# Kernel optimization log

Measured on AMD Instinct MI355X. Metric: run time of the kernel, lower is better.

Reference implementation:

```python
import jax, jax.numpy as jnp
import numpy as np

N = 100000
E = 1600000
IN_C, HID, HEADS, OUT_C = 128, 64, 4, 2
NEG_SLOPE = 0.2


def setup_inputs() -> dict:
    key = jax.random.key(0)
    ks = jax.random.split(key, 10)
    def glorot(k, shape):
        fan = shape[0] + shape[-1]
        return jax.random.uniform(k, shape, jnp.float32, -1.0, 1.0) * np.sqrt(6.0 / fan)
    x = jax.random.normal(ks[0], (N, IN_C), jnp.float32)
    edge_index = jax.random.randint(ks[1], (2, E), 0, N, jnp.int64)
    return {
        "x": x,
        "edge_index": edge_index,
        "W1": glorot(ks[2], (IN_C, HID)),
        "b1": jnp.zeros((HID,), jnp.float32),
        "W2": glorot(ks[3], (HID, HEADS * HID)),
        "att_src": glorot(ks[4], (HEADS, HID)) ,
        "att_dst": glorot(ks[5], (HEADS, HID)),
        "b2": jnp.zeros((HEADS * HID,), jnp.float32),
        "W3": glorot(ks[6], (HEADS * HID, OUT_C)),
        "b3": jnp.zeros((OUT_C,), jnp.float32),
    }


def _add_self_loops(edge_index, n):
    loop = jnp.arange(n, dtype=edge_index.dtype)
    src = jnp.concatenate([edge_index[0], loop])
    dst = jnp.concatenate([edge_index[1], loop])
    return src, dst


def gcn_conv(x, W, b, src, dst, n):
    # x' = X W, then symmetric deg-normalized scatter-add (self-loops included)
    xw = x @ W
    deg = jax.ops.segment_sum(jnp.ones_like(dst, dtype=xw.dtype), dst, num_segments=n)
    dinv = jnp.where(deg > 0, jax.lax.rsqrt(deg), 0.0)
    norm = dinv[src] * dinv[dst]                      # [E2]
    out = jax.ops.segment_sum(xw[src] * norm[:, None], dst, num_segments=n)
    return out + b


def gat_conv(x, W, att_src, att_dst, b, src, dst, n, heads, ch):
    xw = (x @ W).reshape(n, heads, ch)                # [N, H, C]
    a_s = (xw * att_src).sum(-1)                      # [N, H]
    a_d = (xw * att_dst).sum(-1)
    e = jax.nn.leaky_relu(a_s[src] + a_d[dst], NEG_SLOPE)   # [E2, H]
    # segment softmax over incoming edges per destination node
    m = jax.ops.segment_max(e, dst, num_segments=n)
    m = jnp.where(jnp.isfinite(m), m, 0.0)
    e = jnp.exp(e - m[dst])
    den = jax.ops.segment_sum(e, dst, num_segments=n)
    alpha = e / (den[dst] + 1e-16)                    # [E2, H]
    out = jax.ops.segment_sum(xw[src] * alpha[:, :, None], dst, num_segments=n)
    return out.reshape(n, heads * ch) + b


def reference(x, edge_index, W1, b1, W2, att_src, att_dst, b2, W3, b3):
    n = x.shape[0]
    src, dst = _add_self_loops(edge_index, n)
    h = jax.nn.relu(gcn_conv(x, W1, b1, src, dst, n))
    h = jax.nn.elu(gat_conv(h, W2, att_src, att_dst, b2, src, dst, n, HEADS, HID))
    return gcn_conv(h, W3, b3, src, dst, n)
```

## Files before the change

kernel.cpp:

```cpp
#include <hip/hip_runtime.h>
#include <math.h>

#define N_NODES 100000
#define N_EDGES 1600000
#define E2      (N_NODES + N_EDGES)
#define IN_C    128
#define HID     64
#define HEADS   4
#define HH      256
#define OUT_C   2
#define NEG_SLOPE 0.2f

#define SB   1024
#define NSB  ((N_NODES + SB - 1) / SB)
#define NRANGE 4
#define RDIV   25000
#define BINS   RDIV
#define BINW   (BINS / 2)
#define NBK    100
#define CHUNK  (N_EDGES / NBK)
#define C4     (CHUNK / 4)
#define CITER4 ((C4 + 255) / 256)
#define NHB    (NRANGE * NBK)
#define NFC    (N_EDGES / 256)
#define RT     10
#define NT1    6250
#define NGEMM1 ((NT1 + 3) / 4)

typedef __attribute__((ext_vector_type(8))) short bf16x8;
typedef __attribute__((ext_vector_type(4))) float f32x4;

__device__ __forceinline__ float bf2f(unsigned short u) {
    return __uint_as_float(((unsigned)u) << 16);
}
__device__ __forceinline__ unsigned short f2bf(float f) {
    unsigned u = __float_as_uint(f);
    u += 0x7fffu + ((u >> 16) & 1u);
    return (unsigned short)(u >> 16);
}


__global__ __launch_bounds__(256) void k_prep(const float* __restrict__ W2,
        const float* __restrict__ W1,
        const float* __restrict__ att_src, const float* __restrict__ att_dst,
        unsigned short* __restrict__ W2t, unsigned short* __restrict__ wsdt,
        unsigned short* __restrict__ W1t) {
    int b = blockIdx.x, t = threadIdx.x;
    if (b < 64) {
        int g = b * 256 + t;
        int k = g >> 8, n = g & 255;
        W2t[n * 64 + k] = f2bf(W2[g]);
        return;
    }
    if (b < 66) {
        int g = (b - 64) * 256 + t;
        wsdt[512 + g] = 0;
        int k = g >> 3, o = g & 7;
        int h = o & 3;
        const float* att = (o < 4) ? att_src : att_dst;
        float acc = 0.f;
        const float* wrow = W2 + (size_t)k * HH + h * 64;
        const float* arow = att + h * 64;
        for (int c = 0; c < 64; ++c) acc = fmaf(wrow[c], arow[c], acc);
        wsdt[o * 64 + k] = f2bf(acc);
        return;
    }
    int g = (b - 66) * 256 + t;
    int k = g >> 6, n = g & 63;
    W1t[n * 128 + k] = f2bf(W1[g]);
}

__global__ __launch_bounds__(256) void k_hist(const int* __restrict__ ei,
        unsigned short* __restrict__ hp16, unsigned short* __restrict__ rank16) {
    __shared__ unsigned int hh[BINW];
    int b = blockIdx.x, t = threadIdx.x;
    int r = b & 3, k = b >> 2;
    for (int i = t; i < BINW; i += 256) hh[i] = 0u;
    __syncthreads();
    const int4* dp4 = (const int4*)(ei + N_EDGES + (size_t)k * CHUNK);
    unsigned short* rp = rank16 + (size_t)k * CHUNK;
    int lo = r * RDIV;
#pragma unroll 2
    for (int it = 0; it < CITER4; ++it) {
        int i4 = it * 256 + t;
        if (i4 < C4) {
            int4 v = dp4[i4];
            int base = i4 * 4;
            int d0 = v.x - lo, d1 = v.y - lo, d2 = v.z - lo, d3 = v.w - lo;
            if ((unsigned)d0 < (unsigned)RDIV) {
                unsigned sh = (d0 & 1) * 16;
                unsigned old = atomicAdd(&hh[d0 >> 1], 1u << sh);
                rp[base + 0] = (unsigned short)(old >> sh);
            }
            if ((unsigned)d1 < (unsigned)RDIV) {
                unsigned sh = (d1 & 1) * 16;
                unsigned old = atomicAdd(&hh[d1 >> 1], 1u << sh);
                rp[base + 1] = (unsigned short)(old >> sh);
            }
            if ((unsigned)d2 < (unsigned)RDIV) {
                unsigned sh = (d2 & 1) * 16;
                unsigned old = atomicAdd(&hh[d2 >> 1], 1u << sh);
                rp[base + 2] = (unsigned short)(old >> sh);
            }
            if ((unsigned)d3 < (unsigned)RDIV) {
                unsigned sh = (d3 & 1) * 16;
                unsigned old = atomicAdd(&hh[d3 >> 1], 1u << sh);
                rp[base + 3] = (unsigned short)(old >> sh);
            }
        }
    }
    __syncthreads();
    unsigned* hp = (unsigned*)(hp16 + (size_t)(r * NBK + k) * BINS);
    for (int i = t; i < BINW; i += 256) hp[i] = hh[i];
}

__global__ __launch_bounds__(256) void k_scan1(unsigned short* __restrict__ hp16,
        int* __restrict__ cnt, int* __restrict__ bsum) {
    int b = blockIdx.x, t = threadIdx.x;
    int s = 0;
#pragma unroll
    for (int u = 0; u < 4; ++u) {
        int i = b * SB + u * 256 + t;
        if (i < N_NODES) {
            int r = i / RDIV, bin = i - r * RDIV;
            unsigned short* p = hp16 + (size_t)r * NBK * BINS + bin;
            unsigned acc = 0;
            for (int k = 0; k < NBK; ++k) {
                unsigned short hv = p[(size_t)k * BINS];
                p[(size_t)k * BINS] = (unsigned short)acc;
                acc += hv;
            }
            cnt[i] = (int)acc;
            s += (int)acc + 1;
        }
    }
#pragma unroll
    for (int off = 1; off < 64; off <<= 1) s += __shfl_xor(s, off);
    __shared__ int wsum[4];
    int lane = t & 63, wv = t >> 6;
    if (lane == 0) wsum[wv] = s;
    __syncthreads();
    if (t == 0) bsum[b] = (wsum[0] + wsum[1]) + (wsum[2] + wsum[3]);
}

__global__ __launch_bounds__(256) void k_scan3(const int* __restrict__ cnt,
        const int* __restrict__ bsum, int* __restrict__ rowptr,
        float* __restrict__ dinv, int* __restrict__ col) {
    int b = blockIdx.x, t = threadIdx.x;
    int lane = t & 63, wv = t >> 6;
    __shared__ int wred[4];
    {
        int v = (t < b) ? bsum[t] : 0;
#pragma unroll
        for (int off = 1; off < 64; off <<= 1) v += __shfl_xor(v, off);
        if (lane == 0) wred[wv] = v;
    }
    __syncthreads();
    int pre = (wred[0] + wred[1]) + (wred[2] + wred[3]);
    __syncthreads();

    int i = b * SB + t * 4;
    int c0 = 0, c1 = 0, c2 = 0, c3 = 0;
    if (i + 3 < N_NODES) {
        int4 v = *(const int4*)(cnt + i);
        c0 = v.x; c1 = v.y; c2 = v.z; c3 = v.w;
    } else if (i < N_NODES) {
        c0 = cnt[i];
        if (i + 1 < N_NODES) c1 = cnt[i + 1];
        if (i + 2 < N_NODES) c2 = cnt[i + 2];
    }
    int n0 = (i < N_NODES), n1 = (i + 1 < N_NODES),
        n2 = (i + 2 < N_NODES), n3 = (i + 3 < N_NODES);
    int d0 = c0 + n0, d1 = c1 + n1, d2 = c2 + n2, d3 = c3 + n3;
    int s = (d0 + d1) + (d2 + d3);
    int inc = s;
#pragma unroll
    for (int off = 1; off < 64; off <<= 1) {
        int u = __shfl_up(inc, off);
        if (lane >= off) inc += u;
    }
    __shared__ int wtot[4];
    if (lane == 63) wtot[wv] = inc;
    __syncthreads();
    int base = pre + (inc - s);
    for (int w = 0; w < wv; ++w) base += wtot[w];
    if (n0) { rowptr[i]     = base;                dinv[i]     = rsqrtf((float)d0); col[base] = i; }
    if (n1) { rowptr[i + 1] = base + d0;           dinv[i + 1] = rsqrtf((float)d1); col[base + d0] = i + 1; }
    if (n2) { rowptr[i + 2] = base + d0 + d1;      dinv[i + 2] = rsqrtf((float)d2); col[base + d0 + d1] = i + 2; }
    if (n3) { rowptr[i + 3] = base + d0 + d1 + d2; dinv[i + 3] = rsqrtf((float)d3); col[base + d0 + d1 + d2] = i + 3; }
    if (b == 0 && t == 0) rowptr[N_NODES] = E2;
}

__global__ __launch_bounds__(256) void k_fillg(const int* __restrict__ ei,
        const int* __restrict__ rowptr, const unsigned short* __restrict__ hp16,
        const unsigned short* __restrict__ rank16, int* __restrict__ col,
        const float* __restrict__ x, const unsigned short* __restrict__ W1t,
        unsigned short* __restrict__ xw1b) {
    int b = blockIdx.x, t = threadIdx.x;
    if (b < NGEMM1) {
        int lane = t & 63, wv = t >> 6;
        int m = lane & 15, quad = lane >> 4;
        bf16x8 B[4][4];
#pragma unroll
        for (int ct = 0; ct < 4; ++ct)
#pragma unroll
            for (int ks = 0; ks < 4; ++ks)
                B[ct][ks] = *(const bf16x8*)(W1t + (size_t)(ct * 16 + m) * IN_C
                                             + ks * 32 + quad * 8);
        int tile = b * 4 + wv;
        if (tile >= NT1) return;
        int rbase = tile * 16;
        const float* xp = x + (size_t)(rbase + m) * IN_C + quad * 8;
        f32x4 c0 = {0.f, 0.f, 0.f, 0.f}, c1 = c0, c2 = c0, c3 = c0;
#pragma unroll
        for (int ks = 0; ks < 4; ++ks) {
            float4 f0 = *(const float4*)(xp + ks * 32);
            float4 f1 = *(const float4*)(xp + ks * 32 + 4);
            bf16x8 a;
            a[0] = (short)f2bf(f0.x); a[1] = (short)f2bf(f0.y);
            a[2] = (short)f2bf(f0.z); a[3] = (short)f2bf(f0.w);
            a[4] = (short)f2bf(f1.x); a[5] = (short)f2bf(f1.y);
            a[6] = (short)f2bf(f1.z); a[7] = (short)f2bf(f1.w);
            c0 = __builtin_amdgcn_mfma_f32_16x16x32_bf16(a, B[0][ks], c0, 0, 0, 0);
            c1 = __builtin_amdgcn_mfma_f32_16x16x32_bf16(a, B[1][ks], c1, 0, 0, 0);
            c2 = __builtin_amdgcn_mfma_f32_16x16x32_bf16(a, B[2][ks], c2, 0, 0, 0);
            c3 = __builtin_amdgcn_mfma_f32_16x16x32_bf16(a, B[3][ks], c3, 0, 0, 0);
        }
        int row0 = rbase + quad * 4;
#pragma unroll
        for (int ct = 0; ct < 4; ++ct) {
            f32x4 c = (ct == 0) ? c0 : (ct == 1) ? c1 : (ct == 2) ? c2 : c3;
            unsigned short* p = xw1b + (size_t)row0 * HID + ct * 16 + m;
#pragma unroll
            for (int r = 0; r < 4; ++r) p[(size_t)r * HID] = f2bf(c[r]);
        }
        return;
    }
    int i = (b - NGEMM1) * 256 + t;
    int d = ei[N_EDGES + i];
    int s = ei[i];
    int r = d / RDIV;
    int bin = d - r * RDIV;
    int k = i / CHUNK;
    unsigned pos = (unsigned)rowptr[d] + 1u
                 + (unsigned)hp16[(size_t)(r * NBK + k) * BINS + bin]
                 + (unsigned)rank16[i];
    col[pos] = s;
}

__global__ __launch_bounds__(256) void k_agg1(const int* __restrict__ rowptr,
        const int* __restrict__ col, const unsigned short* __restrict__ xw1b,
        const float* __restrict__ dinv, const float* __restrict__ b1,
        unsigned short* __restrict__ h1b) {
    int t = threadIdx.x;
    int lane = t & 63;
    int d = blockIdx.x * 4 + (t >> 6);
    if (d >= N_NODES) return;
    int start = rowptr[d], end = rowptr[d + 1];
    int sub = lane >> 4;
    int cpos = lane & 15;
    float4 acc = make_float4(0.f, 0.f, 0.f, 0.f);
    for (int base = start; base < end; base += 64) {
        int cnt = min(64, end - base);
        int sl = (base + lane < end) ? col[base + lane] : 0;
#pragma unroll 2
        for (int j = 0; j < cnt; j += 4) {
            int idx = j + sub;
            int sj = __shfl(sl, idx);
            if (idx < cnt) {
                float di = dinv[sj];
                ushort4 v = ((const ushort4*)(xw1b + (size_t)sj * HID))[cpos];
                acc.x = fmaf(di, bf2f(v.x), acc.x);
                acc.y = fmaf(di, bf2f(v.y), acc.y);
                acc.z = fmaf(di, bf2f(v.z), acc.z);
                acc.w = fmaf(di, bf2f(v.w), acc.w);
            }
        }
    }
    acc.x += __shfl_xor(acc.x, 16); acc.y += __shfl_xor(acc.y, 16);
    acc.z += __shfl_xor(acc.z, 16); acc.w += __shfl_xor(acc.w, 16);
    acc.x += __shfl_xor(acc.x, 32); acc.y += __shfl_xor(acc.y, 32);
    acc.z += __shfl_xor(acc.z, 32); acc.w += __shfl_xor(acc.w, 32);
    if (lane < 16) {
        float di = dinv[d];
        float4 b = ((const float4*)b1)[lane];
        float ox = fmaf(acc.x, di, b.x); ox = ox > 0.f ? ox : 0.f;
        float oy = fmaf(acc.y, di, b.y); oy = oy > 0.f ? oy : 0.f;
        float oz = fmaf(acc.z, di, b.z); oz = oz > 0.f ? oz : 0.f;
        float ow = fmaf(acc.w, di, b.w); ow = ow > 0.f ? ow : 0.f;
        ushort4 o = make_ushort4(f2bf(ox), f2bf(oy), f2bf(oz), f2bf(ow));
        ((ushort4*)(h1b + (size_t)d * HID))[lane] = o;
    }
}

__global__ __launch_bounds__(256) void k_attn(const unsigned short* __restrict__ h1b,
        const unsigned short* __restrict__ wsdt,
        float* __restrict__ a_s, float* __restrict__ a_d) {
    int t = threadIdx.x;
    int lane = t & 63, wv = t >> 6;
    int m = lane & 15, quad = lane >> 4;
    bf16x8 Bw0 = *(const bf16x8*)(wsdt + (size_t)m * 64 + quad * 8);
    bf16x8 Bw1 = *(const bf16x8*)(wsdt + (size_t)m * 64 + 32 + quad * 8);
    int tile = blockIdx.x * 4 + wv;
    if (tile >= NT1) return;
    int rbase = tile * 16;
    const unsigned short* ap = h1b + (size_t)(rbase + m) * 64 + quad * 8;
    bf16x8 a0 = *(const bf16x8*)(ap);
    bf16x8 a1 = *(const bf16x8*)(ap + 32);
    f32x4 aw = {0.f, 0.f, 0.f, 0.f};
    aw = __builtin_amdgcn_mfma_f32_16x16x32_bf16(a0, Bw0, aw, 0, 0, 0);
    aw = __builtin_amdgcn_mfma_f32_16x16x32_bf16(a1, Bw1, aw, 0, 0, 0);
    int row = rbase + quad * 4;
    if (m < 4) {
#pragma unroll
        for (int r = 0; r < 4; ++r) a_s[(row + r) * 4 + m] = aw[r];
    } else if (m < 8) {
#pragma unroll
        for (int r = 0; r < 4; ++r) a_d[(row + r) * 4 + (m - 4)] = aw[r];
    }
}

__global__ __launch_bounds__(256) void k_agg2u(const int* __restrict__ rowptr,
        const int* __restrict__ col, const unsigned short* __restrict__ h1b,
        const float* __restrict__ a_s, const float* __restrict__ a_d,
        unsigned short* __restrict__ ub, int dbase) {
    __shared__ int   ss[4][64];
    __shared__ float sp[4][64][4];
    int t = threadIdx.x;
    int lane = t & 63, wv = t >> 6;
    int d = dbase + blockIdx.x * 4 + wv;
    if (d >= N_NODES) return;
    const float4* as4 = (const float4*)a_s;
    float4 adv = ((const float4*)a_d)[d];
    int start = rowptr[d], end = rowptr[d + 1];

    float den0 = 0.f, den1 = 0.f, den2 = 0.f, den3 = 0.f;
    float acc0 = 0.f, acc1 = 0.f, acc2 = 0.f, acc3 = 0.f;
    for (int base = start; base < end; base += 64) {
        int cnt = min(64, end - base);
        float p0 = 0.f, p1 = 0.f, p2 = 0.f, p3 = 0.f;
        int s = 0;
        if (lane < cnt) {
            s = col[base + lane];
            float4 av = as4[s];
            float v;
            v = av.x + adv.x; v = v > 0.f ? v : NEG_SLOPE * v; p0 = __expf(v);
            v = av.y + adv.y; v = v > 0.f ? v : NEG_SLOPE * v; p1 = __expf(v);
            v = av.z + adv.z; v = v > 0.f ? v : NEG_SLOPE * v; p2 = __expf(v);
            v = av.w + adv.w; v = v > 0.f ? v : NEG_SLOPE * v; p3 = __expf(v);
            den0 += p0; den1 += p1; den2 += p2; den3 += p3;
        }
        ss[wv][lane] = s;
        ((float4*)sp[wv])[lane] = make_float4(p0, p1, p2, p3);
#pragma unroll 4
        for (int j = 0; j < cnt; ++j) {
            int sj = ss[wv][j];
            float4 pj = ((const float4*)sp[wv])[j];
            float v = bf2f(h1b[(unsigned)sj * 64u + (unsigned)lane]);
            acc0 = fmaf(pj.x, v, acc0);
            acc1 = fmaf(pj.y, v, acc1);
            acc2 = fmaf(pj.z, v, acc2);
            acc3 = fmaf(pj.w, v, acc3);
        }
    }
#pragma unroll
    for (int mk = 1; mk < 64; mk <<= 1) {
        den0 += __shfl_xor(den0, mk);
        den1 += __shfl_xor(den1, mk);
        den2 += __shfl_xor(den2, mk);
        den3 += __shfl_xor(den3, mk);
    }
    float u0 = acc0 / (den0 + 1e-16f);
    float u1 = acc1 / (den1 + 1e-16f);
    float u2 = acc2 / (den2 + 1e-16f);
    float u3 = acc3 / (den3 + 1e-16f);
    unsigned short* up = ub + (size_t)d * HH;
    up[lane]       = f2bf(u0);
    up[64 + lane]  = f2bf(u1);
    up[128 + lane] = f2bf(u2);
    up[192 + lane] = f2bf(u3);
}

__global__ __launch_bounds__(256) void k_gemm3m(const unsigned short* __restrict__ ub,
        const unsigned short* __restrict__ W2t, const float* __restrict__ b2,
        const float* __restrict__ W3, const float* __restrict__ dinv,
        float2* __restrict__ xw3) {
    int t = threadIdx.x;
    int lane = t & 63, wv = t >> 6;
    int m = lane & 15, quad = lane >> 4;
    int nb = wv * 64 + m;
    bf16x8 B[4][2];
#pragma unroll
    for (int ct = 0; ct < 4; ++ct)
#pragma unroll
        for (int ks = 0; ks < 2; ++ks)
            B[ct][ks] = *(const bf16x8*)(W2t + (size_t)(nb + ct * 16) * 64
                                         + ks * 32 + quad * 8);
    float bv[4]; float2 w3v[4];
#pragma unroll
    for (int ct = 0; ct < 4; ++ct) {
        int n = nb + ct * 16;
        bv[ct] = b2[n];
        w3v[ct] = ((const float2*)W3)[n];
    }
    __shared__ float red[4][16][2];
    int r0 = blockIdx.x * (RT * 16);
    for (int tile = 0; tile < RT; ++tile) {
        int rbase = r0 + tile * 16;
        const unsigned short* ap = ub + (size_t)(rbase + m) * HH + wv * 64 + quad * 8;
        bf16x8 a0 = *(const bf16x8*)(ap);
        bf16x8 a1 = *(const bf16x8*)(ap + 32);
        f32x4 c0 = {0.f, 0.f, 0.f, 0.f}, c1 = c0, c2 = c0, c3 = c0;
        c0 = __builtin_amdgcn_mfma_f32_16x16x32_bf16(a0, B[0][0], c0, 0, 0, 0);
        c1 = __builtin_amdgcn_mfma_f32_16x16x32_bf16(a0, B[1][0], c1, 0, 0, 0);
        c2 = __builtin_amdgcn_mfma_f32_16x16x32_bf16(a0, B[2][0], c2, 0, 0, 0);
        c3 = __builtin_amdgcn_mfma_f32_16x16x32_bf16(a0, B[3][0], c3, 0, 0, 0);
        c0 = __builtin_amdgcn_mfma_f32_16x16x32_bf16(a1, B[0][1], c0, 0, 0, 0);
        c1 = __builtin_amdgcn_mfma_f32_16x16x32_bf16(a1, B[1][1], c1, 0, 0, 0);
        c2 = __builtin_amdgcn_mfma_f32_16x16x32_bf16(a1, B[2][1], c2, 0, 0, 0);
        c3 = __builtin_amdgcn_mfma_f32_16x16x32_bf16(a1, B[3][1], c3, 0, 0, 0);
        float px[4] = {0.f, 0.f, 0.f, 0.f}, py[4] = {0.f, 0.f, 0.f, 0.f};
#pragma unroll
        for (int ct = 0; ct < 4; ++ct) {
            f32x4 c = (ct == 0) ? c0 : (ct == 1) ? c1 : (ct == 2) ? c2 : c3;
#pragma unroll
            for (int r = 0; r < 4; ++r) {
                float o = c[r] + bv[ct];
                o = o > 0.f ? o : expm1f(o);
                px[r] = fmaf(o, w3v[ct].x, px[r]);
                py[r] = fmaf(o, w3v[ct].y, py[r]);
            }
        }
#pragma unroll
        for (int mk = 1; mk < 16; mk <<= 1) {
#pragma unroll
            for (int r = 0; r < 4; ++r) {
                px[r] += __shfl_xor(px[r], mk);
                py[r] += __shfl_xor(py[r], mk);
            }
        }
        if (m == 0) {
#pragma unroll
            for (int r = 0; r < 4; ++r) {
                red[wv][quad * 4 + r][0] = px[r];
                red[wv][quad * 4 + r][1] = py[r];
            }
        }
        __syncthreads();
        if (t < 32) {
            int row = t >> 1, xy = t & 1;
            float s = red[0][row][xy] + red[1][row][xy]
                    + red[2][row][xy] + red[3][row][xy];
            ((float*)(xw3 + (rbase + row)))[xy] = s * dinv[rbase + row];
        }
        __syncthreads();
    }
}

__global__ __launch_bounds__(256) void k_agg3(const int* __restrict__ rowptr,
        const int* __restrict__ col, const float2* __restrict__ xw3,
        const float* __restrict__ dinv, const float* __restrict__ b3,
        float* __restrict__ out) {
    int t = threadIdx.x;
    int lane = t & 63;
    int g = lane >> 2, s = lane & 3;
    int d = blockIdx.x * 64 + (t >> 6) * 16 + g;
    if (d >= N_NODES) return;
    int e0 = rowptr[d], e1 = rowptr[d + 1];
    float a0 = 0.f, a1 = 0.f;
    for (int e = e0 + s; e < e1; e += 4) {
        float2 v = xw3[col[e]];
        a0 += v.x; a1 += v.y;
    }
    a0 += __shfl_xor(a0, 1); a1 += __shfl_xor(a1, 1);
    a0 += __shfl_xor(a0, 2); a1 += __shfl_xor(a1, 2);
    if (s == 0) {
        float di = dinv[d];
        out[d * 2 + 0] = fmaf(a0, di, b3[0]);
        out[d * 2 + 1] = fmaf(a1, di, b3[1]);
    }
}


extern "C" void kernel_launch(void* const* d_in, const int* in_sizes, int n_in,
                              void* d_out, int out_size, void* d_ws, size_t ws_size,
                              hipStream_t stream) {
    const float* x       = (const float*)d_in[0];
    const int*   ei      = (const int*)d_in[1];
    const float* W1      = (const float*)d_in[2];
    const float* b1      = (const float*)d_in[3];
    const float* W2      = (const float*)d_in[4];
    const float* att_src = (const float*)d_in[5];
    const float* att_dst = (const float*)d_in[6];
    const float* b2      = (const float*)d_in[7];
    const float* W3      = (const float*)d_in[8];
    const float* b3      = (const float*)d_in[9];
    float* out = (float*)d_out;
    (void)in_sizes; (void)n_in; (void)out_size; (void)ws_size;

    char* ws = (char*)d_ws;
    size_t off = 0;
    auto alloc = [&](size_t bytes) -> void* {
        void* p = ws + off;
        off = (off + bytes + 255) & ~(size_t)255;
        return p;
    };
    int*    rowptr = (int*)alloc((N_NODES + 1) * sizeof(int));
    int*    cnt    = (int*)alloc(N_NODES * sizeof(int));
    int*    bsum   = (int*)alloc(NSB * sizeof(int));
    int*    col    = (int*)alloc((size_t)E2 * sizeof(int));
    float*  dinv   = (float*)alloc(N_NODES * sizeof(float));
    unsigned short* W2t  = (unsigned short*)alloc(64 * 256 * sizeof(unsigned short));
    unsigned short* wsdt = (unsigned short*)alloc(16 * 64 * sizeof(unsigned short));
    unsigned short* W1t  = (unsigned short*)alloc(64 * 128 * sizeof(unsigned short));
    unsigned short* xw1b = (unsigned short*)alloc((size_t)N_NODES * HID * sizeof(unsigned short));
    unsigned short* h1b  = (unsigned short*)alloc((size_t)N_NODES * HID * sizeof(unsigned short));
    float*  a_s    = (float*)alloc((size_t)N_NODES * HEADS * sizeof(float));
    float*  a_d    = (float*)alloc((size_t)N_NODES * HEADS * sizeof(float));
    unsigned short* ub   = (unsigned short*)alloc((size_t)N_NODES * HH * sizeof(unsigned short));
    float2* xw3    = (float2*)alloc((size_t)N_NODES * sizeof(float2));
    unsigned short* hp16   = ub;
    unsigned short* rank16 = ub + (size_t)NHB * BINS;

    k_prep<<<98, 256, 0, stream>>>(W2, W1, att_src, att_dst, W2t, wsdt, W1t);
    k_hist<<<NHB, 256, 0, stream>>>(ei, hp16, rank16);
    k_scan1<<<NSB, 256, 0, stream>>>(hp16, cnt, bsum);
    k_scan3<<<NSB, 256, 0, stream>>>(cnt, bsum, rowptr, dinv, col);
    k_fillg<<<NGEMM1 + NFC, 256, 0, stream>>>(ei, rowptr, hp16, rank16,
                                              col, x, W1t, xw1b);

    k_agg1<<<(N_NODES + 3) / 4, 256, 0, stream>>>(rowptr, col, xw1b, dinv, b1, h1b);
    k_attn<<<(NT1 + 3) / 4, 256, 0, stream>>>(h1b, wsdt, a_s, a_d);
    const int HALF = 50000;
    k_agg2u<<<HALF / 4, 256, 0, stream>>>(rowptr, col, h1b, a_s, a_d, ub, 0);
    k_agg2u<<<(N_NODES - HALF + 3) / 4, 256, 0, stream>>>(rowptr, col, h1b, a_s, a_d, ub, HALF);
    k_gemm3m<<<(N_NODES / 16) / RT, 256, 0, stream>>>(ub, W2t, b2, W3, dinv, xw3);
    k_agg3<<<(N_NODES + 63) / 64, 256, 0, stream>>>(rowptr, col, xw3, dinv, b3, out);
}
```

Measured before the change: 370.9 us.

## Move GEMM1 into scan kernel and vectorize GAT aggregation gathers

After: 387.4 us. 1.04x slower.

```diff
diff --git a/kernel.cpp b/kernel.cpp
--- a/kernel.cpp
+++ b/kernel.cpp
@@ -114,90 +114,12 @@
     for (int i = t; i < BINW; i += 256) hp[i] = hh[i];
 }
 
-__global__ __launch_bounds__(256) void k_scan1(unsigned short* __restrict__ hp16,
-        int* __restrict__ cnt, int* __restrict__ bsum) {
-    int b = blockIdx.x, t = threadIdx.x;
-    int s = 0;
-#pragma unroll
-    for (int u = 0; u < 4; ++u) {
-        int i = b * SB + u * 256 + t;
-        if (i < N_NODES) {
-            int r = i / RDIV, bin = i - r * RDIV;
-            unsigned short* p = hp16 + (size_t)r * NBK * BINS + bin;
-            unsigned acc = 0;
-            for (int k = 0; k < NBK; ++k) {
-                unsigned short hv = p[(size_t)k * BINS];
-                p[(size_t)k * BINS] = (unsigned short)acc;
-                acc += hv;
-            }
-            cnt[i] = (int)acc;
-            s += (int)acc + 1;
-        }
-    }
-#pragma unroll
-    for (int off = 1; off < 64; off <<= 1) s += __shfl_xor(s, off);
-    __shared__ int wsum[4];
-    int lane = t & 63, wv = t >> 6;
-    if (lane == 0) wsum[wv] = s;
-    __syncthreads();
-    if (t == 0) bsum[b] = (wsum[0] + wsum[1]) + (wsum[2] + wsum[3]);
-}
-
-__global__ __launch_bounds__(256) void k_scan3(const int* __restrict__ cnt,
-        const int* __restrict__ bsum, int* __restrict__ rowptr,
-        float* __restrict__ dinv, int* __restrict__ col) {
-    int b = blockIdx.x, t = threadIdx.x;
-    int lane = t & 63, wv = t >> 6;
-    __shared__ int wred[4];
-    {
-        int v = (t < b) ? bsum[t] : 0;
-#pragma unroll
-        for (int off = 1; off < 64; off <<= 1) v += __shfl_xor(v, off);
-        if (lane == 0) wred[wv] = v;
-    }
-    __syncthreads();
-    int pre = (wred[0] + wred[1]) + (wred[2] + wred[3]);
-    __syncthreads();
-
-    int i = b * SB + t * 4;
-    int c0 = 0, c1 = 0, c2 = 0, c3 = 0;
-    if (i + 3 < N_NODES) {
-        int4 v = *(const int4*)(cnt + i);
-        c0 = v.x; c1 = v.y; c2 = v.z; c3 = v.w;
-    } else if (i < N_NODES) {
-        c0 = cnt[i];
-        if (i + 1 < N_NODES) c1 = cnt[i + 1];
-        if (i + 2 < N_NODES) c2 = cnt[i + 2];
-    }
-    int n0 = (i < N_NODES), n1 = (i + 1 < N_NODES),
-        n2 = (i + 2 < N_NODES), n3 = (i + 3 < N_NODES);
-    int d0 = c0 + n0, d1 = c1 + n1, d2 = c2 + n2, d3 = c3 + n3;
-    int s = (d0 + d1) + (d2 + d3);
-    int inc = s;
-#pragma unroll
-    for (int off = 1; off < 64; off <<= 1) {
-        int u = __shfl_up(inc, off);
-        if (lane >= off) inc += u;
-    }
-    __shared__ int wtot[4];
-    if (lane == 63) wtot[wv] = inc;
-    __syncthreads();
-    int base = pre + (inc - s);
-    for (int w = 0; w < wv; ++w) base += wtot[w];
-    if (n0) { rowptr[i]     = base;                dinv[i]     = rsqrtf((float)d0); col[base] = i; }
-    if (n1) { rowptr[i + 1] = base + d0;           dinv[i + 1] = rsqrtf((float)d1); col[base + d0] = i + 1; }
-    if (n2) { rowptr[i + 2] = base + d0 + d1;      dinv[i + 2] = rsqrtf((float)d2); col[base + d0 + d1] = i + 2; }
-    if (n3) { rowptr[i + 3] = base + d0 + d1 + d2; dinv[i + 3] = rsqrtf((float)d3); col[base + d0 + d1 + d2] = i + 3; }
-    if (b == 0 && t == 0) rowptr[N_NODES] = E2;
-}
-
-__global__ __launch_bounds__(256) void k_fillg(const int* __restrict__ ei,
-        const int* __restrict__ rowptr, const unsigned short* __restrict__ hp16,
-        const unsigned short* __restrict__ rank16, int* __restrict__ col,
+__global__ __launch_bounds__(256) void k_scan1g(unsigned short* __restrict__ hp16,
+        int* __restrict__ cnt, int* __restrict__ bsum,
         const float* __restrict__ x, const unsigned short* __restrict__ W1t,
         unsigned short* __restrict__ xw1b) {
     int b = blockIdx.x, t = threadIdx.x;
-    if (b < NGEMM1) {
+    if (b >= NSB) {
         int lane = t & 63, wv = t >> 6;
         int m = lane & 15, quad = lane >> 4;
         bf16x8 B[4][4];
@@ -207,7 +129,7 @@
             for (int ks = 0; ks < 4; ++ks)
                 B[ct][ks] = *(const bf16x8*)(W1t + (size_t)(ct * 16 + m) * IN_C
                                              + ks * 32 + quad * 8);
-        int tile = b * 4 + wv;
+        int tile = (b - NSB) * 4 + wv;
         if (tile >= NT1) return;
         int rbase = tile * 16;
         const float* xp = x + (size_t)(rbase + m) * IN_C + quad * 8;
@@ -236,7 +158,84 @@
         }
         return;
     }
-    int i = (b - NGEMM1) * 256 + t;
+    int s = 0;
+#pragma unroll
+    for (int u = 0; u < 4; ++u) {
+        int i = b * SB + u * 256 + t;
+        if (i < N_NODES) {
+            int r = i / RDIV, bin = i - r * RDIV;
+            unsigned short* p = hp16 + (size_t)r * NBK * BINS + bin;
+            unsigned acc = 0;
+            for (int k = 0; k < NBK; ++k) {
+                unsigned short hv = p[(size_t)k * BINS];
+                p[(size_t)k * BINS] = (unsigned short)acc;
+                acc += hv;
+            }
+            cnt[i] = (int)acc;
+            s += (int)acc + 1;
+        }
+    }
+#pragma unroll
+    for (int off = 1; off < 64; off <<= 1) s += __shfl_xor(s, off);
+    __shared__ int wsum[4];
+    int lane = t & 63, wv = t >> 6;
+    if (lane == 0) wsum[wv] = s;
+    __syncthreads();
+    if (t == 0) bsum[b] = (wsum[0] + wsum[1]) + (wsum[2] + wsum[3]);
+}
+
+__global__ __launch_bounds__(256) void k_scan3(const int* __restrict__ cnt,
+        const int* __restrict__ bsum, int* __restrict__ rowptr,
+        float* __restrict__ dinv, int* __restrict__ col) {
+    int b = blockIdx.x, t = threadIdx.x;
+    int lane = t & 63, wv = t >> 6;
+    __shared__ int wred[4];
+    {
+        int v = (t < b) ? bsum[t] : 0;
+#pragma unroll
+        for (int off = 1; off < 64; off <<= 1) v += __shfl_xor(v, off);
+        if (lane == 0) wred[wv] = v;
+    }
+    __syncthreads();
+    int pre = (wred[0] + wred[1]) + (wred[2] + wred[3]);
+    __syncthreads();
+
+    int i = b * SB + t * 4;
+    int c0 = 0, c1 = 0, c2 = 0, c3 = 0;
+    if (i + 3 < N_NODES) {
+        int4 v = *(const int4*)(cnt + i);
+        c0 = v.x; c1 = v.y; c2 = v.z; c3 = v.w;
+    } else if (i < N_NODES) {
+        c0 = cnt[i];
+        if (i + 1 < N_NODES) c1 = cnt[i + 1];
+        if (i + 2 < N_NODES) c2 = cnt[i + 2];
+    }
+    int n0 = (i < N_NODES), n1 = (i + 1 < N_NODES),
+        n2 = (i + 2 < N_NODES), n3 = (i + 3 < N_NODES);
+    int d0 = c0 + n0, d1 = c1 + n1, d2 = c2 + n2, d3 = c3 + n3;
+    int s = (d0 + d1) + (d2 + d3);
+    int inc = s;
+#pragma unroll
+    for (int off = 1; off < 64; off <<= 1) {
+        int u = __shfl_up(inc, off);
+        if (lane >= off) inc += u;
+    }
+    __shared__ int wtot[4];
+    if (lane == 63) wtot[wv] = inc;
+    __syncthreads();
+    int base = pre + (inc - s);
+    for (int w = 0; w < wv; ++w) base += wtot[w];
+    if (n0) { rowptr[i]     = base;                dinv[i]     = rsqrtf((float)d0); col[base] = i; }
+    if (n1) { rowptr[i + 1] = base + d0;           dinv[i + 1] = rsqrtf((float)d1); col[base + d0] = i + 1; }
+    if (n2) { rowptr[i + 2] = base + d0 + d1;      dinv[i + 2] = rsqrtf((float)d2); col[base + d0 + d1] = i + 2; }
+    if (n3) { rowptr[i + 3] = base + d0 + d1 + d2; dinv[i + 3] = rsqrtf((float)d3); col[base + d0 + d1 + d2] = i + 3; }
+    if (b == 0 && t == 0) rowptr[N_NODES] = E2;
+}
+
+__global__ void k_fill(const int* __restrict__ ei, const int* __restrict__ rowptr,
+        const unsigned short* __restrict__ hp16,
+        const unsigned short* __restrict__ rank16, int* __restrict__ col) {
+    int i = blockIdx.x * 256 + threadIdx.x;
     int d = ei[N_EDGES + i];
     int s = ei[i];
     int r = d / RDIV;
@@ -328,6 +327,8 @@
     __shared__ float sp[4][64][4];
     int t = threadIdx.x;
     int lane = t & 63, wv = t >> 6;
+    int sub = lane >> 4;
+    int cpos = lane & 15;
     int d = dbase + blockIdx.x * 4 + wv;
     if (d >= N_NODES) return;
     const float4* as4 = (const float4*)a_s;
@@ -335,7 +336,8 @@
     int start = rowptr[d], end = rowptr[d + 1];
 
     float den0 = 0.f, den1 = 0.f, den2 = 0.f, den3 = 0.f;
-    float acc0 = 0.f, acc1 = 0.f, acc2 = 0.f, acc3 = 0.f;
+    float4 A0 = make_float4(0.f, 0.f, 0.f, 0.f);
+    float4 A1 = A0, A2 = A0, A3 = A0;
     for (int base = start; base < end; base += 64) {
         int cnt = min(64, end - base);
         float p0 = 0.f, p1 = 0.f, p2 = 0.f, p3 = 0.f;
@@ -352,15 +354,24 @@
         }
         ss[wv][lane] = s;
         ((float4*)sp[wv])[lane] = make_float4(p0, p1, p2, p3);
-#pragma unroll 4
-        for (int j = 0; j < cnt; ++j) {
-            int sj = ss[wv][j];
-            float4 pj = ((const float4*)sp[wv])[j];
-            float v = bf2f(h1b[(unsigned)sj * 64u + (unsigned)lane]);
-            acc0 = fmaf(pj.x, v, acc0);
-            acc1 = fmaf(pj.y, v, acc1);
-            acc2 = fmaf(pj.z, v, acc2);
-            acc3 = fmaf(pj.w, v, acc3);
+#pragma unroll 2
+        for (int j = 0; j < cnt; j += 4) {
+            int idx = j + sub;
+            if (idx < cnt) {
+                int sj = ss[wv][idx];
+                float4 pj = ((const float4*)sp[wv])[idx];
+                ushort4 v = ((const ushort4*)(h1b + (size_t)sj * 64u))[cpos];
+                float c0 = bf2f(v.x), c1 = bf2f(v.y);
+                float c2 = bf2f(v.z), c3 = bf2f(v.w);
+                A0.x = fmaf(pj.x, c0, A0.x); A0.y = fmaf(pj.x, c1, A0.y);
+                A0.z = fmaf(pj.x, c2, A0.z); A0.w = fmaf(pj.x, c3, A0.w);
+                A1.x = fmaf(pj.y, c0, A1.x); A1.y = fmaf(pj.y, c1, A1.y);
+                A1.z = fmaf(pj.y, c2, A1.z); A1.w = fmaf(pj.y, c3, A1.w);
+                A2.x = fmaf(pj.z, c0, A2.x); A2.y = fmaf(pj.z, c1, A2.y);
+                A2.z = fmaf(pj.z, c2, A2.z); A2.w = fmaf(pj.z, c3, A2.w);
+                A3.x = fmaf(pj.w, c0, A3.x); A3.y = fmaf(pj.w, c1, A3.y);
+                A3.z = fmaf(pj.w, c2, A3.z); A3.w = fmaf(pj.w, c3, A3.w);
+            }
         }
     }
 #pragma unroll
@@ -370,15 +381,30 @@
         den2 += __shfl_xor(den2, mk);
         den3 += __shfl_xor(den3, mk);
     }
-    float u0 = acc0 / (den0 + 1e-16f);
-    float u1 = acc1 / (den1 + 1e-16f);
-    float u2 = acc2 / (den2 + 1e-16f);
-    float u3 = acc3 / (den3 + 1e-16f);
-    unsigned short* up = ub + (size_t)d * HH;
-    up[lane]       = f2bf(u0);
-    up[64 + lane]  = f2bf(u1);
-    up[128 + lane] = f2bf(u2);
-    up[192 + lane] = f2bf(u3);
+#pragma unroll
+    for (int mk = 16; mk < 64; mk <<= 1) {
+        A0.x += __shfl_xor(A0.x, mk); A0.y += __shfl_xor(A0.y, mk);
+        A0.z += __shfl_xor(A0.z, mk); A0.w += __shfl_xor(A0.w, mk);
+        A1.x += __shfl_xor(A1.x, mk); A1.y += __shfl_xor(A1.y, mk);
+        A1.z += __shfl_xor(A1.z, mk); A1.w += __shfl_xor(A1.w, mk);
+        A2.x += __shfl_xor(A2.x, mk); A2.y += __shfl_xor(A2.y, mk);
+        A2.z += __shfl_xor(A2.z, mk); A2.w += __shfl_xor(A2.w, mk);
+        A3.x += __shfl_xor(A3.x, mk); A3.y += __shfl_xor(A3.y, mk);
+        A3.z += __shfl_xor(A3.z, mk); A3.w += __shfl_xor(A3.w, mk);
+    }
+    if (lane < 16) {
+        float r0 = 1.f / (den0 + 1e-16f), r1 = 1.f / (den1 + 1e-16f);
+        float r2 = 1.f / (den2 + 1e-16f), r3 = 1.f / (den3 + 1e-16f);
+        unsigned short* up = ub + (size_t)d * HH;
+        ((ushort4*)(up))[cpos] = make_ushort4(
+            f2bf(A0.x * r0), f2bf(A0.y * r0), f2bf(A0.z * r0), f2bf(A0.w * r0));
+        ((ushort4*)(up + 64))[cpos] = make_ushort4(
+            f2bf(A1.x * r1), f2bf(A1.y * r1), f2bf(A1.z * r1), f2bf(A1.w * r1));
+        ((ushort4*)(up + 128))[cpos] = make_ushort4(
+            f2bf(A2.x * r2), f2bf(A2.y * r2), f2bf(A2.z * r2), f2bf(A2.w * r2));
+        ((ushort4*)(up + 192))[cpos] = make_ushort4(
+            f2bf(A3.x * r3), f2bf(A3.y * r3), f2bf(A3.z * r3), f2bf(A3.w * r3));
+    }
 }
 
 __global__ __launch_bounds__(256) void k_gemm3m(const unsigned short* __restrict__ ub,
@@ -524,10 +550,9 @@
 
     k_prep<<<98, 256, 0, stream>>>(W2, W1, att_src, att_dst, W2t, wsdt, W1t);
     k_hist<<<NHB, 256, 0, stream>>>(ei, hp16, rank16);
-    k_scan1<<<NSB, 256, 0, stream>>>(hp16, cnt, bsum);
+    k_scan1g<<<NSB + NGEMM1, 256, 0, stream>>>(hp16, cnt, bsum, x, W1t, xw1b);
     k_scan3<<<NSB, 256, 0, stream>>>(cnt, bsum, rowptr, dinv, col);
-    k_fillg<<<NGEMM1 + NFC, 256, 0, stream>>>(ei, rowptr, hp16, rank16,
-                                              col, x, W1t, xw1b);
+    k_fill<<<NFC, 256, 0, stream>>>(ei, rowptr, hp16, rank16, col);
 
     k_agg1<<<(N_NODES + 3) / 4, 256, 0, stream>>>(rowptr, col, xw1b, dinv, b1, h1b);
     k_attn<<<(NT1 + 3) / 4, 256, 0, stream>>>(h1b, wsdt, a_s, a_d);
```

## Pre-scale GEMM1 rows by dinv and fuse attention scores into aggregation

Applied to the files above, without the earlier changes.

Result: no change. 374.1 us (+0.9%).

```diff
diff --git a/kernel.cpp b/kernel.cpp
--- a/kernel.cpp
+++ b/kernel.cpp
@@ -191,52 +191,54 @@
     if (b == 0 && t == 0) rowptr[N_NODES] = E2;
 }
 
-__global__ __launch_bounds__(256) void k_fillg(const int* __restrict__ ei,
-        const int* __restrict__ rowptr, const unsigned short* __restrict__ hp16,
-        const unsigned short* __restrict__ rank16, int* __restrict__ col,
-        const float* __restrict__ x, const unsigned short* __restrict__ W1t,
+__global__ __launch_bounds__(256) void k_gemm1d(const float* __restrict__ x,
+        const unsigned short* __restrict__ W1t, const float* __restrict__ dinv,
         unsigned short* __restrict__ xw1b) {
-    int b = blockIdx.x, t = threadIdx.x;
-    if (b < NGEMM1) {
-        int lane = t & 63, wv = t >> 6;
-        int m = lane & 15, quad = lane >> 4;
-        bf16x8 B[4][4];
-#pragma unroll
-        for (int ct = 0; ct < 4; ++ct)
-#pragma unroll
-            for (int ks = 0; ks < 4; ++ks)
-                B[ct][ks] = *(const bf16x8*)(W1t + (size_t)(ct * 16 + m) * IN_C
-                                             + ks * 32 + quad * 8);
-        int tile = b * 4 + wv;
-        if (tile >= NT1) return;
-        int rbase = tile * 16;
-        const float* xp = x + (size_t)(rbase + m) * IN_C + quad * 8;
-        f32x4 c0 = {0.f, 0.f, 0.f, 0.f}, c1 = c0, c2 = c0, c3 = c0;
-#pragma unroll
-        for (int ks = 0; ks < 4; ++ks) {
-            float4 f0 = *(const float4*)(xp + ks * 32);
-            float4 f1 = *(const float4*)(xp + ks * 32 + 4);
-            bf16x8 a;
-            a[0] = (short)f2bf(f0.x); a[1] = (short)f2bf(f0.y);
-            a[2] = (short)f2bf(f0.z); a[3] = (short)f2bf(f0.w);
-            a[4] = (short)f2bf(f1.x); a[5] = (short)f2bf(f1.y);
-            a[6] = (short)f2bf(f1.z); a[7] = (short)f2bf(f1.w);
-            c0 = __builtin_amdgcn_mfma_f32_16x16x32_bf16(a, B[0][ks], c0, 0, 0, 0);
-            c1 = __builtin_amdgcn_mfma_f32_16x16x32_bf16(a, B[1][ks], c1, 0, 0, 0);
-            c2 = __builtin_amdgcn_mfma_f32_16x16x32_bf16(a, B[2][ks], c2, 0, 0, 0);
-            c3 = __builtin_amdgcn_mfma_f32_16x16x32_bf16(a, B[3][ks], c3, 0, 0, 0);
-        }
-        int row0 = rbase + quad * 4;
-#pragma unroll
-        for (int ct = 0; ct < 4; ++ct) {
-            f32x4 c = (ct == 0) ? c0 : (ct == 1) ? c1 : (ct == 2) ? c2 : c3;
-            unsigned short* p = xw1b + (size_t)row0 * HID + ct * 16 + m;
-#pragma unroll
-            for (int r = 0; r < 4; ++r) p[(size_t)r * HID] = f2bf(c[r]);
-        }
-        return;
-    }
-    int i = (b - NGEMM1) * 256 + t;
+    int t = threadIdx.x;
+    int lane = t & 63, wv = t >> 6;
+    int m = lane & 15, quad = lane >> 4;
+    bf16x8 B[4][4];
+#pragma unroll
+    for (int ct = 0; ct < 4; ++ct)
+#pragma unroll
+        for (int ks = 0; ks < 4; ++ks)
+            B[ct][ks] = *(const bf16x8*)(W1t + (size_t)(ct * 16 + m) * IN_C
+                                         + ks * 32 + quad * 8);
+    int tile = blockIdx.x * 4 + wv;
+    if (tile >= NT1) return;
+    int rbase = tile * 16;
+    const float* xp = x + (size_t)(rbase + m) * IN_C + quad * 8;
+    f32x4 c0 = {0.f, 0.f, 0.f, 0.f}, c1 = c0, c2 = c0, c3 = c0;
+#pragma unroll
+    for (int ks = 0; ks < 4; ++ks) {
+        float4 f0 = *(const float4*)(xp + ks * 32);
+        float4 f1 = *(const float4*)(xp + ks * 32 + 4);
+        bf16x8 a;
+        a[0] = (short)f2bf(f0.x); a[1] = (short)f2bf(f0.y);
+        a[2] = (short)f2bf(f0.z); a[3] = (short)f2bf(f0.w);
+        a[4] = (short)f2bf(f1.x); a[5] = (short)f2bf(f1.y);
+        a[6] = (short)f2bf(f1.z); a[7] = (short)f2bf(f1.w);
+        c0 = __builtin_amdgcn_mfma_f32_16x16x32_bf16(a, B[0][ks], c0, 0, 0, 0);
+        c1 = __builtin_amdgcn_mfma_f32_16x16x32_bf16(a, B[1][ks], c1, 0, 0, 0);
+        c2 = __builtin_amdgcn_mfma_f32_16x16x32_bf16(a, B[2][ks], c2, 0, 0, 0);
+        c3 = __builtin_amdgcn_mfma_f32_16x16x32_bf16(a, B[3][ks], c3, 0, 0, 0);
+    }
+    int row0 = rbase + quad * 4;
+    float4 dv = *(const float4*)(dinv + row0);
+    float dr[4] = {dv.x, dv.y, dv.z, dv.w};
+#pragma unroll
+    for (int ct = 0; ct < 4; ++ct) {
+        f32x4 c = (ct == 0) ? c0 : (ct == 1) ? c1 : (ct == 2) ? c2 : c3;
+        unsigned short* p = xw1b + (size_t)row0 * HID + ct * 16 + m;
+#pragma unroll
+        for (int r = 0; r < 4; ++r) p[(size_t)r * HID] = f2bf(c[r] * dr[r]);
+    }
+}
+
+__global__ void k_fill(const int* __restrict__ ei, const int* __restrict__ rowptr,
+        const unsigned short* __restrict__ hp16,
+        const unsigned short* __restrict__ rank16, int* __restrict__ col) {
+    int i = blockIdx.x * 256 + threadIdx.x;
     int d = ei[N_EDGES + i];
     int s = ei[i];
     int r = d / RDIV;
@@ -248,10 +250,12 @@
     col[pos] = s;
 }
 
-__global__ __launch_bounds__(256) void k_agg1(const int* __restrict__ rowptr,
+__global__ __launch_bounds__(256) void k_agg1a(const int* __restrict__ rowptr,
         const int* __restrict__ col, const unsigned short* __restrict__ xw1b,
         const float* __restrict__ dinv, const float* __restrict__ b1,
-        unsigned short* __restrict__ h1b) {
+        const unsigned short* __restrict__ wsdt,
+        unsigned short* __restrict__ h1b,
+        float* __restrict__ a_s, float* __restrict__ a_d) {
     int t = threadIdx.x;
     int lane = t & 63;
     int d = blockIdx.x * 4 + (t >> 6);
@@ -268,12 +272,11 @@
             int idx = j + sub;
             int sj = __shfl(sl, idx);
             if (idx < cnt) {
-                float di = dinv[sj];
                 ushort4 v = ((const ushort4*)(xw1b + (size_t)sj * HID))[cpos];
-                acc.x = fmaf(di, bf2f(v.x), acc.x);
-                acc.y = fmaf(di, bf2f(v.y), acc.y);
-                acc.z = fmaf(di, bf2f(v.z), acc.z);
-                acc.w = fmaf(di, bf2f(v.w), acc.w);
+                acc.x += bf2f(v.x);
+                acc.y += bf2f(v.y);
+                acc.z += bf2f(v.z);
+                acc.w += bf2f(v.w);
             }
         }
     }
@@ -281,42 +284,31 @@
     acc.z += __shfl_xor(acc.z, 16); acc.w += __shfl_xor(acc.w, 16);
     acc.x += __shfl_xor(acc.x, 32); acc.y += __shfl_xor(acc.y, 32);
     acc.z += __shfl_xor(acc.z, 32); acc.w += __shfl_xor(acc.w, 32);
-    if (lane < 16) {
-        float di = dinv[d];
-        float4 b = ((const float4*)b1)[lane];
-        float ox = fmaf(acc.x, di, b.x); ox = ox > 0.f ? ox : 0.f;
-        float oy = fmaf(acc.y, di, b.y); oy = oy > 0.f ? oy : 0.f;
-        float oz = fmaf(acc.z, di, b.z); oz = oz > 0.f ? oz : 0.f;
-        float ow = fmaf(acc.w, di, b.w); ow = ow > 0.f ? ow : 0.f;
-        ushort4 o = make_ushort4(f2bf(ox), f2bf(oy), f2bf(oz), f2bf(ow));
-        ((ushort4*)(h1b + (size_t)d * HID))[lane] = o;
-    }
-}
-
-__global__ __launch_bounds__(256) void k_attn(const unsigned short* __restrict__ h1b,
-        const unsigned short* __restrict__ wsdt,
-        float* __restrict__ a_s, float* __restrict__ a_d) {
-    int t = threadIdx.x;
-    int lane = t & 63, wv = t >> 6;
-    int m = lane & 15, quad = lane >> 4;
-    bf16x8 Bw0 = *(const bf16x8*)(wsdt + (size_t)m * 64 + quad * 8);
-    bf16x8 Bw1 = *(const bf16x8*)(wsdt + (size_t)m * 64 + 32 + quad * 8);
-    int tile = blockIdx.x * 4 + wv;
-    if (tile >= NT1) return;
-    int rbase = tile * 16;
-    const unsigned short* ap = h1b + (size_t)(rbase + m) * 64 + quad * 8;
-    bf16x8 a0 = *(const bf16x8*)(ap);
-    bf16x8 a1 = *(const bf16x8*)(ap + 32);
-    f32x4 aw = {0.f, 0.f, 0.f, 0.f};
-    aw = __builtin_amdgcn_mfma_f32_16x16x32_bf16(a0, Bw0, aw, 0, 0, 0);
-    aw = __builtin_amdgcn_mfma_f32_16x16x32_bf16(a1, Bw1, aw, 0, 0, 0);
-    int row = rbase + quad * 4;
-    if (m < 4) {
-#pragma unroll
-        for (int r = 0; r < 4; ++r) a_s[(row + r) * 4 + m] = aw[r];
-    } else if (m < 8) {
-#pragma unroll
-        for (int r = 0; r < 4; ++r) a_d[(row + r) * 4 + (m - 4)] = aw[r];
+    float di = dinv[d];
+    float4 b = ((const float4*)b1)[cpos];
+    float h0 = fmaf(acc.x, di, b.x); h0 = h0 > 0.f ? h0 : 0.f;
+    float h1 = fmaf(acc.y, di, b.y); h1 = h1 > 0.f ? h1 : 0.f;
+    float h2 = fmaf(acc.z, di, b.z); h2 = h2 > 0.f ? h2 : 0.f;
+    float h3 = fmaf(acc.w, di, b.w); h3 = h3 > 0.f ? h3 : 0.f;
+    ushort4 o = make_ushort4(f2bf(h0), f2bf(h1), f2bf(h2), f2bf(h3));
+    if (lane < 16)
+        ((ushort4*)(h1b + (size_t)d * HID))[cpos] = o;
+    float r0 = bf2f(o.x), r1 = bf2f(o.y), r2 = bf2f(o.z), r3 = bf2f(o.w);
+    int hsel = lane >> 4;
+    ushort4 ws = ((const ushort4*)(wsdt + hsel * 64))[cpos];
+    ushort4 wd = ((const ushort4*)(wsdt + (hsel + 4) * 64))[cpos];
+    float ps = r0 * bf2f(ws.x) + r1 * bf2f(ws.y)
+             + r2 * bf2f(ws.z) + r3 * bf2f(ws.w);
+    float pd = r0 * bf2f(wd.x) + r1 * bf2f(wd.y)
+             + r2 * bf2f(wd.z) + r3 * bf2f(wd.w);
+#pragma unroll
+    for (int mk = 1; mk < 16; mk <<= 1) {
+        ps += __shfl_xor(ps, mk);
+        pd += __shfl_xor(pd, mk);
+    }
+    if (cpos == 0) {
+        a_s[d * 4 + hsel] = ps;
+        a_d[d * 4 + hsel] = pd;
     }
 }
 
@@ -526,11 +518,11 @@
     k_hist<<<NHB, 256, 0, stream>>>(ei, hp16, rank16);
     k_scan1<<<NSB, 256, 0, stream>>>(hp16, cnt, bsum);
     k_scan3<<<NSB, 256, 0, stream>>>(cnt, bsum, rowptr, dinv, col);
-    k_fillg<<<NGEMM1 + NFC, 256, 0, stream>>>(ei, rowptr, hp16, rank16,
-                                              col, x, W1t, xw1b);
-
-    k_agg1<<<(N_NODES + 3) / 4, 256, 0, stream>>>(rowptr, col, xw1b, dinv, b1, h1b);
-    k_attn<<<(NT1 + 3) / 4, 256, 0, stream>>>(h1b, wsdt, a_s, a_d);
+    k_gemm1d<<<NGEMM1, 256, 0, stream>>>(x, W1t, dinv, xw1b);
+    k_fill<<<NFC, 256, 0, stream>>>(ei, rowptr, hp16, rank16, col);
+
+    k_agg1a<<<(N_NODES + 3) / 4, 256, 0, stream>>>(rowptr, col, xw1b, dinv, b1,
+                                                   wsdt, h1b, a_s, a_d);
     const int HALF = 50000;
     k_agg2u<<<HALF / 4, 256, 0, stream>>>(rowptr, col, h1b, a_s, a_d, ub, 0);
     k_agg2u<<<(N_NODES - HALF + 3) / 4, 256, 0, stream>>>(rowptr, col, h1b, a_s, a_d, ub, HALF);
```
